# Kernel tuning notes

Measured on AMD Instinct MI355X. Metric: run time of the kernel, lower is better.

Reference implementation:

```python
import jax, jax.numpy as jnp
import numpy as np

SCALE = 0.25  # matches torch forward default scale=1/4 (static: determines output shape)


def _cubic(x):
    # MATLAB bicubic kernel, a = -0.5
    a = np.abs(x)
    a2 = a * a
    a3 = a2 * a
    c1 = (a <= 1).astype(np.float32)
    c2 = ((a > 1) & (a <= 2)).astype(np.float32)
    return (1.5 * a3 - 2.5 * a2 + 1.0) * c1 + (-0.5 * a3 + 2.5 * a2 - 4.0 * a + 2.0) * c2


def _contrib_1d(in_len, out_len, scale):
    # Faithful numpy port of bicubic_imresize.contribute for one axis.
    kw = 4.0 / scale if scale < 1 else 4.0
    x = np.arange(1, out_len + 1, dtype=np.float32)
    u = x / scale + 0.5 * (1.0 - 1.0 / scale)
    left = np.floor(u - kw / 2.0)
    P = int(np.ceil(kw) + 2)
    ind = left[:, None] + np.arange(P, dtype=np.float32)[None, :]   # [out_len, P]
    mid = u[:, None] - ind
    w = scale * _cubic(mid * scale) if scale < 1 else _cubic(mid)
    w = w / w.sum(axis=1, keepdims=True)
    ind = np.clip(ind, 1.0, float(in_len))
    kill = (w[0] == 0)  # torch prunes columns where the FIRST row weight is zero
    w = w[:, ~kill].astype(np.float32)
    idx = ind[:, ~kill].astype(np.int64) - 1  # 0-based
    return w, idx


def setup_inputs() -> dict:
    key = jax.random.key(0)
    return {"input": jax.random.normal(key, (8, 3, 1024, 1024), dtype=jnp.float32)}


def reference(input):
    b, c, h, w_in = input.shape
    oh, ow = int(h * SCALE), int(w_in * SCALE)
    w0_np, i0_np = _contrib_1d(h, oh, SCALE)      # rows: [oh, P0]
    w1_np, i1_np = _contrib_1d(w_in, ow, SCALE)   # cols: [ow, P1]
    w0 = jnp.asarray(w0_np)
    w1 = jnp.asarray(w1_np)
    i0 = jnp.asarray(i0_np)
    i1 = jnp.asarray(i1_np)
    # vertical pass: gather rows then weighted reduce over taps
    rows = input[:, :, i0, :]                          # [b, c, oh, P0, w_in]
    tmp = jnp.einsum('bcopw,op->bcow', rows, w0)       # [b, c, oh, w_in]
    # horizontal pass
    cols = tmp[:, :, :, i1]                            # [b, c, oh, ow, P1]
    out = jnp.einsum('bcowp,wp->bcow', cols, w1)       # [b, c, oh, ow]
    return out
```

## Files before the change

### kernel.cpp

```cpp
#include <hip/hip_runtime.h>

#define IN_H 1024
#define IN_W 1024
#define OUT_H 256
#define OUT_W 256
#define G 8
#define ROWS (4*G + 12)
#define GUARD_L 6
#define PITCH 1040

__constant__ float WTAP[16] = {
    -0.001708984375f, -0.010986328125f, -0.018310546875f, -0.011962890625f,
     0.022705078125f,  0.097412109375f,  0.181884765625f,  0.240966796875f,
     0.240966796875f,  0.181884765625f,  0.097412109375f,  0.022705078125f,
    -0.011962890625f, -0.018310546875f, -0.010986328125f, -0.001708984375f
};

__global__ __launch_bounds__(256, 3)
void bicubic_fused_kernel(const float* __restrict__ in, float* __restrict__ out) {
    const int t   = threadIdx.x;
    const int bc  = blockIdx.x / (OUT_H / G);
    const int og  = blockIdx.x % (OUT_H / G);
    const int oh0 = og * G;

    __shared__ float vrow[G][PITCH];

    const float* src = in + (size_t)bc * IN_H * IN_W;

    float4 acc[G];
#pragma unroll
    for (int i = 0; i < G; ++i) acc[i] = make_float4(0.f, 0.f, 0.f, 0.f);

#pragma unroll
    for (int r = 0; r < ROWS; ++r) {
        int y = oh0 * 4 + r - 6;
        y = min(max(y, 0), IN_H - 1);
        const float4 v = *(const float4*)(src + (size_t)y * IN_W + 4 * t);
#pragma unroll
        for (int i = 0; i < G; ++i) {
            const int j = r - 4 * i;
            if (j >= 0 && j < 16) {
                const float w = WTAP[j];
                acc[i].x = fmaf(w, v.x, acc[i].x);
                acc[i].y = fmaf(w, v.y, acc[i].y);
                acc[i].z = fmaf(w, v.z, acc[i].z);
                acc[i].w = fmaf(w, v.w, acc[i].w);
            }
        }
    }

#pragma unroll
    for (int i = 0; i < G; ++i) {
        float2* p = (float2*)&vrow[i][GUARD_L + 4 * t];
        p[0] = make_float2(acc[i].x, acc[i].y);
        p[1] = make_float2(acc[i].z, acc[i].w);
    }
    if (t == 0) {
#pragma unroll
        for (int i = 0; i < G; ++i)
            for (int k = 0; k < GUARD_L; ++k) vrow[i][k] = acc[i].x;
    }
    if (t == 255) {
#pragma unroll
        for (int i = 0; i < G; ++i)
            for (int k = GUARD_L + IN_W; k < PITCH; ++k) vrow[i][k] = acc[i].w;
    }
    __syncthreads();

#pragma unroll
    for (int i = 0; i < G; ++i) {
        const float4* q = (const float4*)&vrow[i][4 * t];
        float s = 0.f;
#pragma unroll
        for (int k = 0; k < 4; ++k) {
            const float4 v = q[k];
            s = fmaf(WTAP[4 * k + 0], v.x, s);
            s = fmaf(WTAP[4 * k + 1], v.y, s);
            s = fmaf(WTAP[4 * k + 2], v.z, s);
            s = fmaf(WTAP[4 * k + 3], v.w, s);
        }
        out[((size_t)bc * OUT_H + oh0 + i) * OUT_W + t] = s;
    }
}

extern "C" void kernel_launch(void* const* d_in, const int* in_sizes, int n_in,
                              void* d_out, int out_size, void* d_ws, size_t ws_size,
                              hipStream_t stream) {
    const float* in = (const float*)d_in[0];
    float* out = (float*)d_out;
    const int nbc = in_sizes[0] / (IN_H * IN_W);
    dim3 grid(nbc * (OUT_H / G));
    dim3 block(256);
    bicubic_fused_kernel<<<grid, block, 0, stream>>>(in, out);
}
```

Before: 147.8 us.

## Double output rows per block, stage horizontal pass in two halves, swizzle blocks

Each block now produces 16 output rows instead of 8, which cuts the redundant 12-row halo reads per output. To keep the shared-memory footprint the same, the horizontal pass runs in two halves of 8 rows with an extra barrier between them. Block indices are swizzled across groups of 8, and launch bounds drop to 2 blocks per SM to allow the larger accumulator array. The trade-off is more registers per thread, lower occupancy and an additional sync.

```diff
diff --git a/kernel.cpp b/kernel.cpp
--- a/kernel.cpp
+++ b/kernel.cpp
@@ -4,10 +4,11 @@
 #define IN_W 1024
 #define OUT_H 256
 #define OUT_W 256
-#define G 8
+#define G 16
 #define ROWS (4*G + 12)
 #define GUARD_L 6
-#define PITCH 1040
+#define PITCH 1036
+#define HROWS 8
 
 __constant__ float WTAP[16] = {
     -0.001708984375f, -0.010986328125f, -0.018310546875f, -0.011962890625f,
@@ -16,16 +17,21 @@
     -0.011962890625f, -0.018310546875f, -0.010986328125f, -0.001708984375f
 };
 
-__global__ __launch_bounds__(256, 3)
+__global__ __launch_bounds__(256, 2)
 void bicubic_fused_kernel(const float* __restrict__ in, float* __restrict__ out) {
-    const int t   = threadIdx.x;
-    const int bc  = blockIdx.x / (OUT_H / G);
-    const int og  = blockIdx.x % (OUT_H / G);
+    const int t = threadIdx.x;
+
+    const int b   = blockIdx.x;
+    const int per = gridDim.x >> 3;
+    const int swz = (b & 7) * per + (b >> 3);
+
+    const int bc  = swz / (OUT_H / G);
+    const int og  = swz % (OUT_H / G);
     const int oh0 = og * G;
 
-    __shared__ float vrow[G][PITCH];
+    __shared__ float vrow[HROWS][PITCH];
 
-    const float* src = in + (size_t)bc * IN_H * IN_W;
+    const float* src = in + (size_t)bc * (IN_H * IN_W);
 
     float4 acc[G];
 #pragma unroll
@@ -50,36 +56,44 @@
     }
 
 #pragma unroll
-    for (int i = 0; i < G; ++i) {
-        float2* p = (float2*)&vrow[i][GUARD_L + 4 * t];
-        p[0] = make_float2(acc[i].x, acc[i].y);
-        p[1] = make_float2(acc[i].z, acc[i].w);
-    }
-    if (t == 0) {
-#pragma unroll
-        for (int i = 0; i < G; ++i)
-            for (int k = 0; k < GUARD_L; ++k) vrow[i][k] = acc[i].x;
-    }
-    if (t == 255) {
-#pragma unroll
-        for (int i = 0; i < G; ++i)
-            for (int k = GUARD_L + IN_W; k < PITCH; ++k) vrow[i][k] = acc[i].w;
-    }
-    __syncthreads();
+    for (int h = 0; h < 2; ++h) {
+        if (h) __syncthreads();
 
 #pragma unroll
-    for (int i = 0; i < G; ++i) {
-        const float4* q = (const float4*)&vrow[i][4 * t];
-        float s = 0.f;
+        for (int k = 0; k < HROWS; ++k) {
+            const int i = h * HROWS + k;
+            float2* p = (float2*)&vrow[k][GUARD_L + 4 * t];
+            p[0] = make_float2(acc[i].x, acc[i].y);
+            p[1] = make_float2(acc[i].z, acc[i].w);
+        }
+        if (t == 0) {
 #pragma unroll
-        for (int k = 0; k < 4; ++k) {
-            const float4 v = q[k];
-            s = fmaf(WTAP[4 * k + 0], v.x, s);
-            s = fmaf(WTAP[4 * k + 1], v.y, s);
-            s = fmaf(WTAP[4 * k + 2], v.z, s);
-            s = fmaf(WTAP[4 * k + 3], v.w, s);
+            for (int k = 0; k < HROWS; ++k)
+                for (int g = 0; g < GUARD_L; ++g)
+                    vrow[k][g] = acc[h * HROWS + k].x;
         }
-        out[((size_t)bc * OUT_H + oh0 + i) * OUT_W + t] = s;
+        if (t == 255) {
+#pragma unroll
+            for (int k = 0; k < HROWS; ++k)
+                for (int g = GUARD_L + IN_W; g < PITCH; ++g)
+                    vrow[k][g] = acc[h * HROWS + k].w;
+        }
+        __syncthreads();
+
+#pragma unroll
+        for (int k = 0; k < HROWS; ++k) {
+            const float4* q = (const float4*)&vrow[k][4 * t];
+            float s = 0.f;
+#pragma unroll
+            for (int m = 0; m < 4; ++m) {
+                const float4 v = q[m];
+                s = fmaf(WTAP[4 * m + 0], v.x, s);
+                s = fmaf(WTAP[4 * m + 1], v.y, s);
+                s = fmaf(WTAP[4 * m + 2], v.z, s);
+                s = fmaf(WTAP[4 * m + 3], v.w, s);
+            }
+            out[((size_t)bc * OUT_H + oh0 + h * HROWS + k) * OUT_W + t] = s;
+        }
     }
 }
 
```

New measurement: 146.9 us. Within noise of the previous version (-0.6%).
